# Kernel tuning notes

Measured on AMD Instinct MI355X. Metric: run time of the kernel, lower is better.

Reference implementation:

```python
import jax, jax.numpy as jnp
import numpy as np

DIM = 64
NUM_FEAT = 14
NUM_OUT = 105
N_NODES = 8192
N_EDGES = 16384
N_GRAPHS = 256
N_STEMS = 2048
N_JBONDS = 1024


def lrelu(v):
    return jax.nn.leaky_relu(v, 0.01)


def setup_inputs() -> dict:
    key = jax.random.key(0)
    ks = jax.random.split(key, 40)
    def rn(k, shape, s=0.1):
        return jax.random.normal(k, shape, dtype=jnp.float32) * s
    inp = {}
    inp['x'] = jax.random.normal(ks[0], (N_NODES, NUM_FEAT), dtype=jnp.float32)
    inp['edge_attr'] = jax.random.uniform(ks[1], (N_EDGES, 4), dtype=jnp.float32)
    inp['edge_index'] = jax.random.randint(ks[2], (2, N_EDGES), 0, N_NODES)
    inp['batch'] = jnp.sort(jax.random.randint(ks[3], (N_NODES,), 0, N_GRAPHS))
    inp['stem_atmidx'] = jax.random.randint(ks[4], (N_STEMS,), 0, N_NODES)
    inp['jbond_atmidx'] = jax.random.randint(ks[5], (N_JBONDS, 2), 0, N_NODES)
    # lin0
    inp['lin0_w'] = rn(ks[6], (NUM_FEAT, DIM)); inp['lin0_b'] = rn(ks[7], (DIM,))
    # NNConv edge net: Linear(4,dim) -> LeakyReLU -> Linear(dim, dim*dim)
    inp['net_w1'] = rn(ks[8], (4, DIM)); inp['net_b1'] = rn(ks[9], (DIM,))
    inp['net_w2'] = rn(ks[10], (DIM, DIM * DIM), 0.02); inp['net_b2'] = rn(ks[11], (DIM * DIM,), 0.02)
    # NNConv root weight + bias
    inp['conv_root'] = rn(ks[12], (DIM, DIM)); inp['conv_bias'] = rn(ks[13], (DIM,))
    # GRU (torch gate order r,z,n); stored [in, 3*dim]
    inp['gru_w_ih'] = rn(ks[14], (DIM, 3 * DIM)); inp['gru_w_hh'] = rn(ks[15], (DIM, 3 * DIM))
    inp['gru_b_ih'] = rn(ks[16], (3 * DIM,)); inp['gru_b_hh'] = rn(ks[17], (3 * DIM,))
    # node2stem MLP
    inp['n2s_w1'] = rn(ks[18], (DIM, DIM)); inp['n2s_b1'] = rn(ks[19], (DIM,))
    inp['n2s_w2'] = rn(ks[20], (DIM, NUM_OUT)); inp['n2s_b2'] = rn(ks[21], (NUM_OUT,))
    # node2jbond MLP
    inp['n2j_w1'] = rn(ks[22], (DIM, DIM)); inp['n2j_b1'] = rn(ks[23], (DIM,))
    inp['n2j_w2'] = rn(ks[24], (DIM, 1)); inp['n2j_b2'] = rn(ks[25], (1,))
    # Set2Set LSTM(2*dim -> dim), torch gate order i,f,g,o; stored [in, 4*dim]
    inp['s2s_w_ih'] = rn(ks[26], (2 * DIM, 4 * DIM)); inp['s2s_w_hh'] = rn(ks[27], (DIM, 4 * DIM))
    inp['s2s_b_ih'] = rn(ks[28], (4 * DIM,)); inp['s2s_b_hh'] = rn(ks[29], (4 * DIM,))
    # lin_out
    inp['lin_out_w'] = rn(ks[30], (2 * DIM, 2)); inp['lin_out_b'] = rn(ks[31], (2,))
    return inp


def reference(x, edge_attr, lin0_w, lin0_b, net_w1, net_b1, net_w2, net_b2,
              conv_root, conv_bias, gru_w_ih, gru_w_hh, gru_b_ih, gru_b_hh,
              n2s_w1, n2s_b1, n2s_w2, n2s_b2, n2j_w1, n2j_b1, n2j_w2, n2j_b2,
              s2s_w_ih, s2s_w_hh, s2s_b_ih, s2s_b_hh, lin_out_w, lin_out_b,
              edge_index, batch, stem_atmidx, jbond_atmidx):
    N = x.shape[0]
    src, dst = edge_index[0], edge_index[1]
    out = lrelu(x @ lin0_w + lin0_b)          # [N, dim]
    h = out
    # edge-conditioned weights (edge_attr is constant across the 6 iterations)
    ew = (lrelu(edge_attr @ net_w1 + net_b1) @ net_w2 + net_b2).reshape(-1, DIM, DIM)  # [E,dim,dim]
    deg = jnp.maximum(jax.ops.segment_sum(jnp.ones_like(dst, dtype=x.dtype), dst, num_segments=N), 1.0)[:, None]
    for _ in range(6):
        msg = jnp.einsum('ei,eio->eo', out[src], ew)                        # per-edge matmul
        agg = jax.ops.segment_sum(msg, dst, num_segments=N) / deg          # scatter-mean
        m = lrelu(agg + out @ conv_root + conv_bias)
        # GRU update (torch gate order r,z,n)
        gi = m @ gru_w_ih + gru_b_ih
        gh = h @ gru_w_hh + gru_b_hh
        ir, iz, inn = jnp.split(gi, 3, axis=-1)
        hr, hz, hn = jnp.split(gh, 3, axis=-1)
        r = jax.nn.sigmoid(ir + hr)
        z = jax.nn.sigmoid(iz + hz)
        n = jnp.tanh(inn + r * hn)
        h = (1.0 - z) * n + z * h
        out = h
    # per-stem block logits
    stem_preds = lrelu(out[stem_atmidx] @ n2s_w1 + n2s_b1) @ n2s_w2 + n2s_b2  # [S, num_out]
    # jbond: gather both endpoints, predict scalar, mean over the pair
    jb = out[jbond_atmidx.reshape(-1)]
    jpred = lrelu(jb @ n2j_w1 + n2j_b1) @ n2j_w2 + n2j_b2                     # [2J,1]
    jbond_preds = jpred.reshape(jbond_atmidx.shape).mean(axis=1)              # [J]
    # Set2Set, processing_steps=1
    B = N_GRAPHS
    hS = jnp.zeros((B, DIM), x.dtype)
    cS = jnp.zeros((B, DIM), x.dtype)
    q_star = jnp.zeros((B, 2 * DIM), x.dtype)
    gates = q_star @ s2s_w_ih + s2s_b_ih + hS @ s2s_w_hh + s2s_b_hh
    gi_, gf_, gg_, go_ = jnp.split(gates, 4, axis=-1)
    cS = jax.nn.sigmoid(gf_) * cS + jax.nn.sigmoid(gi_) * jnp.tanh(gg_)
    hS = jax.nn.sigmoid(go_) * jnp.tanh(cS)
    q = hS                                                                    # [B, dim]
    e = jnp.sum(out * q[batch], axis=-1)                                      # [N]
    emax = jax.ops.segment_max(e, batch, num_segments=B)
    a_un = jnp.exp(e - emax[batch])
    a = a_un / jax.ops.segment_sum(a_un, batch, num_segments=B)[batch]
    r_pool = jax.ops.segment_sum(a[:, None] * out, batch, num_segments=B)     # [B, dim]
    q_star = jnp.concatenate([q, r_pool], axis=1)                             # [B, 2*dim]
    scalar_outs = q_star @ lin_out_w + lin_out_b                              # [B, 2]
    return (scalar_outs, stem_preds, jbond_preds)
```

## Files before the change

kernel.cpp:

```cpp
#include <hip/hip_runtime.h>

#define DIM 64
#define NF 14
#define NOUT 105
#define NN 8192
#define NE 16384
#define NB 256
#define NS 2048
#define NJ 1024
#define KTOT 4160

#define C_X      0
#define C_EA     114688
#define C_L0W    180224
#define C_L0B    181120
#define C_NW1    181184
#define C_NB1    181440
#define C_NW2    181504
#define C_NB2    443648
#define C_CRT    447744
#define C_CB     451840
#define C_GWIH   451904
#define C_GWHH   464192
#define C_GBIH   476480
#define C_GBHH   476672
#define C_SW1    476864
#define C_SB1    480960
#define C_SW2    481024
#define C_SB2    487744
#define C_JW1    487856
#define C_JB1    491952
#define C_JW2    492016
#define C_JB2    492080
#define C_S2IH   492088
#define C_S2HH   492344
#define C_LOW    492600
#define C_LOB    492856
#define C_TOT    492864

typedef float f32x4 __attribute__((ext_vector_type(4)));
typedef short bf16x8 __attribute__((ext_vector_type(8)));

__device__ __forceinline__ float bf2f(unsigned short u){
  union { unsigned int i; float f; } v; v.i = ((unsigned int)u) << 16; return v.f;
}
__device__ __forceinline__ unsigned short f2bf(float f){
  union { float f; unsigned int i; } v; v.f = f;
  unsigned int x = v.i;
  return (unsigned short)((x + 0x7FFFu + ((x >> 16) & 1u)) >> 16);
}
__device__ __forceinline__ float sigm(float x){ return 1.f / (1.f + __expf(-x)); }
__device__ __forceinline__ float tanh_f(float x){
  x = fminf(10.f, fmaxf(-10.f, x));
  float e = __expf(2.f * x);
  return (e - 1.f) / (e + 1.f);
}
__device__ __forceinline__ float lrelu(float x){ return x > 0.f ? x : 0.01f * x; }

__device__ __forceinline__ float wred_sum(float v){
  #pragma unroll
  for (int off = 32; off > 0; off >>= 1) v += __shfl_xor(v, off, 64);
  return v;
}
__device__ __forceinline__ float wred_max(float v){
  #pragma unroll
  for (int off = 32; off > 0; off >>= 1) v = fmaxf(v, __shfl_xor(v, off, 64));
  return v;
}


__global__ void k_detect(const unsigned short* __restrict__ ea, int* __restrict__ flag){
  __shared__ int cnt;
  if (threadIdx.x == 0) cnt = 0;
  __syncthreads();
  int c = 0;
  for (int i = threadIdx.x; i < 8192; i += 256) c += (ea[2*i] >> 15) & 1;
  atomicAdd(&cnt, c);
  __syncthreads();
  if (threadIdx.x == 0) *flag = (cnt > 100) ? 1 : 0;
}

struct CvtArgs {
  const void* src[26];
  int n[26];
  int off[26];
};

__global__ void k_cvt(CvtArgs a, const int* __restrict__ flag, unsigned short* __restrict__ dst){
  bool f32 = (*flag != 0);
  int gid = blockIdx.x * blockDim.x + threadIdx.x, gs = gridDim.x * blockDim.x;
  #pragma unroll 1
  for (int j = 0; j < 26; ++j){
    const void* s = a.src[j];
    int n = a.n[j], o = a.off[j];
    for (int i = gid; i < n; i += gs)
      dst[o + i] = f32 ? f2bf(((const float*)s)[i]) : ((const unsigned short*)s)[i];
  }
}

#define SETUP_BLOCKS 7249

__global__ __launch_bounds__(256) void k_setup(const unsigned short* __restrict__ cvt,
                       const int* __restrict__ ei,
                       float* __restrict__ deg,
                       float* __restrict__ actF, unsigned short* __restrict__ actB,
                       unsigned short* __restrict__ z,
                       unsigned short* __restrict__ w2rt,
                       unsigned short* __restrict__ crt, unsigned short* __restrict__ btg,
                       float* __restrict__ cbg, float* __restrict__ qv){
  int bid = blockIdx.x, tid = threadIdx.x;
  if (bid < 2048){
    const unsigned short* x = cvt + C_X;
    const unsigned short* w = cvt + C_L0W;
    const unsigned short* b = cvt + C_L0B;
    int idx = bid * 256 + tid;
    int n = idx >> 6, d = idx & 63;
    float acc = bf2f(b[d]);
    #pragma unroll
    for (int f = 0; f < NF; ++f) acc += bf2f(x[n*NF + f]) * bf2f(w[f*DIM + d]);
    float v = lrelu(acc);
    actF[idx] = v; actB[idx] = f2bf(v);
  } else if (bid < 6144){
    const unsigned short* ea = cvt + C_EA;
    const unsigned short* w  = cvt + C_NW1;
    const unsigned short* b  = cvt + C_NB1;
    int idx = (bid - 2048) * 256 + tid;
    int e = idx >> 6, d = idx & 63;
    float acc = bf2f(b[d]);
    #pragma unroll
    for (int f = 0; f < 4; ++f) acc += bf2f(ea[e*4 + f]) * bf2f(w[f*DIM + d]);
    z[idx] = f2bf(lrelu(acc));
  } else if (bid < 7184){
    int idx = (bid - 6144) * 256 + tid;
    const unsigned short* w2 = cvt + C_NW2;
    const unsigned short* b2 = cvt + C_NB2;
    int o = idx / KTOT, k = idx - o * KTOT;
    w2rt[idx] = (k < 4096) ? w2[(k >> 6) * 4096 + (k & 63) * 64 + o]
                           : b2[(k - 4096) * 64 + o];
  } else if (bid < 7248){
    int e = (bid - 7184) * 256 + tid;
    if (e < NE) atomicAdd(&deg[ei[NE + e]], 1.0f);
  } else {
    const unsigned short* cr  = cvt + C_CRT;
    const unsigned short* wih = cvt + C_GWIH;
    const unsigned short* whh = cvt + C_GWHH;
    const unsigned short* bih = cvt + C_GBIH;
    const unsigned short* bhh = cvt + C_GBHH;
    const unsigned short* s2sbih = cvt + C_S2IH;
    const unsigned short* s2sbhh = cvt + C_S2HH;
    for (int t = tid; t < 4096; t += 256){ int n = t & 63, k = t >> 6; crt[n*64 + k] = cr[k*64 + n]; }
    for (int t = tid; t < 32768; t += 256){
      int nidx = t >> 7, kidx = t & 127;
      int g = nidx >> 6, d = nidx & 63, ki = kidx & 63;
      unsigned short v = 0;
      if (kidx < 64){
        if (g == 0) v = wih[ki*192 + d];
        else if (g == 1) v = wih[ki*192 + 64 + d];
        else if (g == 2) v = wih[ki*192 + 128 + d];
      } else {
        if (g == 0) v = whh[ki*192 + d];
        else if (g == 1) v = whh[ki*192 + 64 + d];
        else if (g == 3) v = whh[ki*192 + 128 + d];
      }
      btg[nidx*128 + kidx] = v;
    }
    if (tid < 256){
      int g = tid >> 6, d = tid & 63;
      float v;
      if (g == 0) v = bf2f(bih[d]) + bf2f(bhh[d]);
      else if (g == 1) v = bf2f(bih[64 + d]) + bf2f(bhh[64 + d]);
      else if (g == 2) v = bf2f(bih[128 + d]);
      else v = bf2f(bhh[128 + d]);
      cbg[tid] = v;
    }
    if (tid < 64){
      float gi = bf2f(s2sbih[tid])       + bf2f(s2sbhh[tid]);
      float gg = bf2f(s2sbih[128 + tid]) + bf2f(s2sbhh[128 + tid]);
      float go = bf2f(s2sbih[192 + tid]) + bf2f(s2sbhh[192 + tid]);
      float c = sigm(gi) * tanh_f(gg);
      qv[tid] = sigm(go) * tanh_f(c);
    }
  }
}


__global__ __launch_bounds__(256) void k_msg(const unsigned short* __restrict__ actB,
                                             const unsigned short* __restrict__ z,
                                             const unsigned short* __restrict__ w2rt,
                                             const int* __restrict__ ei,
                                             float* __restrict__ agg){
  __shared__ float smsg[4 * 2048];
  int tid = threadIdx.x;
  int w = tid >> 6, lane = tid & 63;
  int lm = lane & 15, q8 = (lane >> 4) * 8;
  int e0  = blockIdx.x * 32;
  int kz0 = w * 16;

  uint4 ap[2][2];
  int rowe[2];
  #pragma unroll
  for (int mt = 0; mt < 2; ++mt){
    rowe[mt] = e0 + mt*16 + lm;
    int srcn = ei[rowe[mt]];
    ap[mt][0] = *(const uint4*)&actB[(size_t)srcn*64 + q8];
    ap[mt][1] = *(const uint4*)&actB[(size_t)srcn*64 + 32 + q8];
  }
  const unsigned short* wrow[4];
  #pragma unroll
  for (int nt = 0; nt < 4; ++nt)
    wrow[nt] = w2rt + (size_t)(nt*16 + lm)*KTOT + q8;

  f32x4 acc[2][4];
  #pragma unroll
  for (int mt = 0; mt < 2; ++mt)
    #pragma unroll
    for (int nt = 0; nt < 4; ++nt) acc[mt][nt] = (f32x4){0.f, 0.f, 0.f, 0.f};

  #pragma unroll 4
  for (int u = 0; u < 16; ++u){
    int kz = kz0 + u;
    float zf[2];
    #pragma unroll
    for (int mt = 0; mt < 2; ++mt)
      zf[mt] = bf2f(z[(size_t)rowe[mt]*64 + kz]);
    #pragma unroll
    for (int h = 0; h < 2; ++h){
      bf16x8 bfr[4];
      #pragma unroll
      for (int nt = 0; nt < 4; ++nt)
        bfr[nt] = *(const bf16x8*)&wrow[nt][kz*64 + h*32];
      #pragma unroll
      for (int mt = 0; mt < 2; ++mt){
        const unsigned int* apw = (const unsigned int*)&ap[mt][h];
        bf16x8 af;
        #pragma unroll
        for (int hh = 0; hh < 4; ++hh){
          float flo = __uint_as_float(apw[hh] << 16) * zf[mt];
          float fhi = __uint_as_float(apw[hh] & 0xFFFF0000u) * zf[mt];
          unsigned int pk;
          asm("v_cvt_pk_bf16_f32 %0, %1, %2" : "=v"(pk) : "v"(flo), "v"(fhi));
          ((unsigned int*)&af)[hh] = pk;
        }
        #pragma unroll
        for (int nt = 0; nt < 4; ++nt)
          acc[mt][nt] = __builtin_amdgcn_mfma_f32_16x16x32_bf16(af, bfr[nt], acc[mt][nt], 0, 0, 0);
      }
    }
  }
  if (w == 3){
    #pragma unroll
    for (int h = 0; h < 2; ++h){
      bf16x8 bfr[4];
      #pragma unroll
      for (int nt = 0; nt < 4; ++nt)
        bfr[nt] = *(const bf16x8*)&wrow[nt][4096 + h*32];
      #pragma unroll
      for (int mt = 0; mt < 2; ++mt){
        bf16x8 af = *(const bf16x8*)&ap[mt][h];
        #pragma unroll
        for (int nt = 0; nt < 4; ++nt)
          acc[mt][nt] = __builtin_amdgcn_mfma_f32_16x16x32_bf16(af, bfr[nt], acc[mt][nt], 0, 0, 0);
      }
    }
  }
  {
    int rq = (lane >> 4) * 4;
    float* slab = &smsg[w * 2048];
    #pragma unroll
    for (int mt = 0; mt < 2; ++mt)
      #pragma unroll
      for (int nt = 0; nt < 4; ++nt)
        #pragma unroll
        for (int r = 0; r < 4; ++r)
          slab[(mt*16 + rq + r)*64 + nt*16 + lm] = acc[mt][nt][r];
  }
  __syncthreads();
  for (int idx = tid; idx < 2048; idx += 256){
    int row = idx >> 6, col = idx & 63;
    float s = smsg[idx] + smsg[idx + 2048] + smsg[idx + 4096] + smsg[idx + 6144];
    atomicAdd(&agg[(size_t)ei[NE + e0 + row]*64 + col], s);
  }
}


__global__ __launch_bounds__(256) void k_gru(const unsigned short* __restrict__ actB_in,
                                             const float* __restrict__ actF_in,
                                             float* __restrict__ agg, const float* __restrict__ deg,
                                             const unsigned short* __restrict__ crt,
                                             const unsigned short* __restrict__ cvt,
                                             const unsigned short* __restrict__ btg,
                                             const float* __restrict__ cbg,
                                             float* __restrict__ actF_out, unsigned short* __restrict__ actB_out){
  const unsigned short* cbias = cvt + C_CB;
  __shared__ __align__(16) unsigned short s_frag[2*4*16*8];
  int w = threadIdx.x >> 6, lane = threadIdx.x & 63;
  int lm = lane & 15, q = lane >> 4;
  int q8 = q*8, rq = q*4;
  int r0 = blockIdx.x * 16;
  f32x4 am = (f32x4){0.f, 0.f, 0.f, 0.f};
  #pragma unroll
  for (int kk = 0; kk < 2; ++kk){
    bf16x8 a = *(const bf16x8*)&actB_in[(size_t)(r0 + lm)*64 + kk*32 + q8];
    bf16x8 b = *(const bf16x8*)&crt[(size_t)(w*16 + lm)*64 + kk*32 + q8];
    am = __builtin_amdgcn_mfma_f32_16x16x32_bf16(a, b, am, 0, 0, 0);
  }
  {
    int col = w*16 + lm;
    float cb = bf2f(cbias[col]);
    int kk2 = w >> 1, q2 = (w & 1)*2 + (lm >> 3), j = lm & 7;
    #pragma unroll
    for (int r = 0; r < 4; ++r){
      int row = r0 + rq + r;
      float dg = fmaxf(deg[row], 1.f);
      float v = am[r] + agg[(size_t)row*64 + col] / dg + cb;
      agg[(size_t)row*64 + col] = 0.f;
      s_frag[((kk2*4 + q2)*16 + (rq + r))*8 + j] = f2bf(lrelu(v));
    }
  }
  __syncthreads();
  f32x4 g[4];
  #pragma unroll
  for (int t = 0; t < 4; ++t) g[t] = (f32x4){0.f, 0.f, 0.f, 0.f};
  #pragma unroll
  for (int kk = 0; kk < 4; ++kk){
    bf16x8 a;
    if (kk < 2) a = *(const bf16x8*)&s_frag[(kk*4 + q)*128 + lm*8];
    else        a = *(const bf16x8*)&actB_in[(size_t)(r0 + lm)*64 + (kk - 2)*32 + q8];
    #pragma unroll
    for (int t = 0; t < 4; ++t){
      bf16x8 b = *(const bf16x8*)&btg[(size_t)(t*64 + w*16 + lm)*128 + kk*32 + q8];
      g[t] = __builtin_amdgcn_mfma_f32_16x16x32_bf16(a, b, g[t], 0, 0, 0);
    }
  }
  {
    int d = w*16 + lm;
    float cb_r = cbg[d], cb_z = cbg[64 + d], cb_n = cbg[128 + d], cb_h = cbg[192 + d];
    #pragma unroll
    for (int r = 0; r < 4; ++r){
      int row = r0 + rq + r;
      float rr = sigm(g[0][r] + cb_r);
      float zz = sigm(g[1][r] + cb_z);
      float nn = tanh_f(g[2][r] + cb_n + rr * (g[3][r] + cb_h));
      float ho = actF_in[(size_t)row*64 + d];
      float hn2 = (1.f - zz) * nn + zz * ho;
      actF_out[(size_t)row*64 + d] = hn2;
      actB_out[(size_t)row*64 + d] = f2bf(hn2);
    }
  }
}


__device__ __forceinline__ int lower_bound_batch(const int* b, int val){
  int lo = 0, hi = NN;
  while (lo < hi){ int mid = (lo + hi) >> 1; if (b[mid] < val) lo = mid + 1; else hi = mid; }
  return lo;
}

__device__ __forceinline__ void store_out(void* outp, const int* flag, size_t idx, float v){
  if (*flag) ((float*)outp)[idx] = v;
  else       ((unsigned short*)outp)[idx] = f2bf(v);
}

__global__ __launch_bounds__(256) void k_heads(const float* __restrict__ act,
                                               const int* __restrict__ batch,
                                               const float* __restrict__ qv,
                                               const int* __restrict__ sidx,
                                               const int* __restrict__ jidx,
                                               const unsigned short* __restrict__ cvt,
                                               const int* __restrict__ flag,
                                               void* __restrict__ outp){
  int bid = blockIdx.x;
  int w = threadIdx.x >> 6, lane = threadIdx.x & 63;
  if (bid < 512){
    const unsigned short* w1 = cvt + C_SW1;
    const unsigned short* b1 = cvt + C_SB1;
    const unsigned short* w2 = cvt + C_SW2;
    const unsigned short* b2 = cvt + C_SB2;
    __shared__ float sa[4][64], st[4][64];
    int s = bid * 4 + w;
    int a = sidx[s];
    sa[w][lane] = act[(size_t)a*64 + lane];
    __syncthreads();
    float t = bf2f(b1[lane]);
    #pragma unroll 8
    for (int i = 0; i < 64; ++i) t += sa[w][i] * bf2f(w1[i*64 + lane]);
    st[w][lane] = lrelu(t);
    __syncthreads();
    size_t base = 512 + (size_t)s * NOUT;
    float v = bf2f(b2[lane]);
    #pragma unroll 8
    for (int d = 0; d < 64; ++d) v += st[w][d] * bf2f(w2[d*NOUT + lane]);
    store_out(outp, flag, base + lane, v);
    int o2 = 64 + lane;
    if (o2 < NOUT){
      float v2 = bf2f(b2[o2]);
      #pragma unroll 8
      for (int d = 0; d < 64; ++d) v2 += st[w][d] * bf2f(w2[d*NOUT + o2]);
      store_out(outp, flag, base + o2, v2);
    }
  } else if (bid < 768){
    const unsigned short* w1 = cvt + C_JW1;
    const unsigned short* b1 = cvt + C_JB1;
    const unsigned short* w2 = cvt + C_JW2;
    const unsigned short* b2 = cvt + C_JB2;
    __shared__ float a0[4][64], a1[4][64];
    int j = (bid - 512) * 4 + w;
    int i0 = jidx[j*2], i1 = jidx[j*2 + 1];
    a0[w][lane] = act[(size_t)i0*64 + lane];
    a1[w][lane] = act[(size_t)i1*64 + lane];
    __syncthreads();
    float t0 = bf2f(b1[lane]), t1 = t0;
    #pragma unroll 8
    for (int i = 0; i < 64; ++i){
      float wv = bf2f(w1[i*64 + lane]);
      t0 += a0[w][i] * wv;
      t1 += a1[w][i] * wv;
    }
    t0 = lrelu(t0); t1 = lrelu(t1);
    float p = (t0 + t1) * bf2f(w2[lane]);
    p = wred_sum(p);
    if (lane == 0) store_out(outp, flag, 512 + (size_t)NS*NOUT + j, 0.5f * p + bf2f(b2[0]));
  } else {
    const unsigned short* lw = cvt + C_LOW;
    const unsigned short* lb = cvt + C_LOB;
    __shared__ float se[4][512];
    int b = (bid - 768) * 4 + w;
    int lo = lower_bound_batch(batch, b);
    int hi = lower_bound_batch(batch, b + 1);
    int cnt = hi - lo; if (cnt > 512) cnt = 512;
    float qvl = qv[lane];
    for (int ii = 0; ii < cnt; ++ii){
      float p = act[(size_t)(lo + ii)*64 + lane] * qvl;
      p = wred_sum(p);
      if (lane == 0) se[w][ii] = p;
    }
    __syncthreads();
    float em = -3.4e38f;
    for (int ii = lane; ii < cnt; ii += 64) em = fmaxf(em, se[w][ii]);
    em = wred_max(em);
    float sm = 0.f;
    for (int ii = lane; ii < cnt; ii += 64) sm += __expf(se[w][ii] - em);
    float denom = wred_sum(sm);
    float rp = 0.f;
    for (int ii = 0; ii < cnt; ++ii) rp += __expf(se[w][ii] - em) * act[(size_t)(lo + ii)*64 + lane];
    if (cnt > 0 && denom > 0.f) rp /= denom;
    float s0 = qvl*bf2f(lw[lane*2])     + rp*bf2f(lw[(64 + lane)*2]);
    float s1 = qvl*bf2f(lw[lane*2 + 1]) + rp*bf2f(lw[(64 + lane)*2 + 1]);
    s0 = wred_sum(s0); s1 = wred_sum(s1);
    if (lane == 0){
      store_out(outp, flag, b*2,     s0 + bf2f(lb[0]));
      store_out(outp, flag, b*2 + 1, s1 + bf2f(lb[1]));
    }
  }
}


extern "C" void kernel_launch(void* const* d_in, const int* in_sizes, int n_in,
                              void* d_out, int out_size, void* d_ws, size_t ws_size,
                              hipStream_t stream){
  (void)in_sizes; (void)n_in; (void)out_size; (void)ws_size;
  const int* edge_index = (const int*)d_in[2];
  const int* batch      = (const int*)d_in[3];
  const int* stem_idx   = (const int*)d_in[4];
  const int* jbond_idx  = (const int*)d_in[5];

  char* ws = (char*)d_ws;
  size_t off = 0;
  auto alloc = [&](size_t bytes) -> void* {
    void* p = ws + off; off += (bytes + 255) & ~(size_t)255; return p;
  };
  unsigned short* cvt  = (unsigned short*)alloc((size_t)C_TOT * 2);
  unsigned short* w2rt = (unsigned short*)alloc((size_t)64 * KTOT * 2);
  unsigned short* z_bf = (unsigned short*)alloc((size_t)NE * 64 * 2);
  float* actF0 = (float*)alloc((size_t)NN * 64 * 4);
  float* actF1 = (float*)alloc((size_t)NN * 64 * 4);
  unsigned short* actB0 = (unsigned short*)alloc((size_t)NN * 64 * 2);
  unsigned short* actB1 = (unsigned short*)alloc((size_t)NN * 64 * 2);
  float* deg  = (float*)alloc(NN * 4);
  float* agg  = (float*)alloc((size_t)NN * 64 * 4);
  unsigned short* crt = (unsigned short*)alloc(64 * 64 * 2);
  unsigned short* btg = (unsigned short*)alloc(256 * 128 * 2);
  float* cbg  = (float*)alloc(256 * 4);
  float* qv   = (float*)alloc(64 * 4);
  int* flag   = (int*)alloc(256);

  hipMemsetAsync(deg, 0, ((size_t)NN * 4) + ((size_t)NN * 64 * 4), stream);

  k_detect<<<1, 256, 0, stream>>>((const unsigned short*)d_in[1], flag);

  CvtArgs ca;
  const int srcIdx[26] = {0,1,6,7,8,9,10,11,12,13,14,15,16,17,18,19,20,21,22,23,24,25,28,29,30,31};
  const int ns[26]  = {114688,65536,896,64,256,64,262144,4096,4096,64,12288,12288,192,192,
                       4096,64,6720,105,4096,64,64,1,256,256,256,2};
  const int ofs[26] = {C_X,C_EA,C_L0W,C_L0B,C_NW1,C_NB1,C_NW2,C_NB2,C_CRT,C_CB,C_GWIH,C_GWHH,
                       C_GBIH,C_GBHH,C_SW1,C_SB1,C_SW2,C_SB2,C_JW1,C_JB1,C_JW2,C_JB2,
                       C_S2IH,C_S2HH,C_LOW,C_LOB};
  for (int j = 0; j < 26; ++j){ ca.src[j] = d_in[srcIdx[j]]; ca.n[j] = ns[j]; ca.off[j] = ofs[j]; }
  k_cvt<<<512, 256, 0, stream>>>(ca, flag, cvt);

  k_setup<<<SETUP_BLOCKS, 256, 0, stream>>>(cvt, edge_index, deg,
                                            actF0, actB0, z_bf, w2rt,
                                            crt, btg, cbg, qv);

  for (int t = 0; t < 6; ++t){
    const float* aF_in  = (t & 1) ? actF1 : actF0;
    float* aF_out       = (t & 1) ? actF0 : actF1;
    const unsigned short* aB_in = (t & 1) ? actB1 : actB0;
    unsigned short* aB_out      = (t & 1) ? actB0 : actB1;
    k_msg<<<NE/32, 256, 0, stream>>>(aB_in, z_bf, w2rt, edge_index, agg);
    k_gru<<<NN/16, 256, 0, stream>>>(aB_in, aF_in, agg, deg, crt, cvt, btg, cbg,
                                     aF_out, aB_out);
  }
  k_heads<<<832, 256, 0, stream>>>(actF0, batch, qv, stem_idx, jbond_idx, cvt, flag, d_out);
}
```

Measured before the change: 515.7 us.

## Pre-swizzle edge-net weights into MFMA fragment order and split K across blocks

The setup kernel now lays out the transposed edge-network weight matrix in MFMA B-fragment order, so each lane loads one contiguous 16-byte chunk per fragment instead of strided rows. The message kernel is also split along the K (z-dimension) axis into two halves per 32-edge group, doubling the grid and halving each block's loop. This targets coalescing of weight loads and adds parallelism and occupancy. The cost is that the two K-halves both write into agg, doubling the scatter and atomic traffic in the epilogue.

Result: faster. 470.4 us (-8.8%).

```diff
diff --git a/kernel.cpp b/kernel.cpp
--- a/kernel.cpp
+++ b/kernel.cpp
@@ -105,7 +105,7 @@
                        float* __restrict__ deg,
                        float* __restrict__ actF, unsigned short* __restrict__ actB,
                        unsigned short* __restrict__ z,
-                       unsigned short* __restrict__ w2rt,
+                       unsigned short* __restrict__ w2f,
                        unsigned short* __restrict__ crt, unsigned short* __restrict__ btg,
                        float* __restrict__ cbg, float* __restrict__ qv){
   int bid = blockIdx.x, tid = threadIdx.x;
@@ -134,9 +134,13 @@
     int idx = (bid - 6144) * 256 + tid;
     const unsigned short* w2 = cvt + C_NW2;
     const unsigned short* b2 = cvt + C_NB2;
-    int o = idx / KTOT, k = idx - o * KTOT;
-    w2rt[idx] = (k < 4096) ? w2[(k >> 6) * 4096 + (k & 63) * 64 + o]
-                           : b2[(k - 4096) * 64 + o];
+    int f = idx >> 9, r = idx & 511;
+    int lane = r >> 3, j = r & 7;
+    int kz = f >> 3, h = (f >> 2) & 1, nt = f & 3;
+    int o = nt*16 + (lane & 15);
+    int k = kz*64 + h*32 + (lane >> 4)*8 + j;
+    w2f[idx] = (k < 4096) ? w2[(k >> 6)*4096 + (k & 63)*64 + o]
+                          : b2[(k - 4096)*64 + o];
   } else if (bid < 7248){
     int e = (bid - 7184) * 256 + tid;
     if (e < NE) atomicAdd(&deg[ei[NE + e]], 1.0f);
@@ -186,15 +190,16 @@
 
 __global__ __launch_bounds__(256) void k_msg(const unsigned short* __restrict__ actB,
                                              const unsigned short* __restrict__ z,
-                                             const unsigned short* __restrict__ w2rt,
+                                             const unsigned short* __restrict__ w2f,
                                              const int* __restrict__ ei,
                                              float* __restrict__ agg){
   __shared__ float smsg[4 * 2048];
   int tid = threadIdx.x;
   int w = tid >> 6, lane = tid & 63;
   int lm = lane & 15, q8 = (lane >> 4) * 8;
-  int e0  = blockIdx.x * 32;
-  int kz0 = w * 16;
+  int g  = blockIdx.x >> 1, kh = blockIdx.x & 1;
+  int e0  = g * 32;
+  int kz0 = kh * 32 + w * 8;
 
   uint4 ap[2][2];
   int rowe[2];
@@ -205,10 +210,6 @@
     ap[mt][0] = *(const uint4*)&actB[(size_t)srcn*64 + q8];
     ap[mt][1] = *(const uint4*)&actB[(size_t)srcn*64 + 32 + q8];
   }
-  const unsigned short* wrow[4];
-  #pragma unroll
-  for (int nt = 0; nt < 4; ++nt)
-    wrow[nt] = w2rt + (size_t)(nt*16 + lm)*KTOT + q8;
 
   f32x4 acc[2][4];
   #pragma unroll
@@ -216,8 +217,8 @@
     #pragma unroll
     for (int nt = 0; nt < 4; ++nt) acc[mt][nt] = (f32x4){0.f, 0.f, 0.f, 0.f};
 
-  #pragma unroll 4
-  for (int u = 0; u < 16; ++u){
+  #pragma unroll 2
+  for (int u = 0; u < 8; ++u){
     int kz = kz0 + u;
     float zf[2];
     #pragma unroll
@@ -228,7 +229,7 @@
       bf16x8 bfr[4];
       #pragma unroll
       for (int nt = 0; nt < 4; ++nt)
-        bfr[nt] = *(const bf16x8*)&wrow[nt][kz*64 + h*32];
+        bfr[nt] = *(const bf16x8*)&w2f[(size_t)(kz*8 + h*4 + nt)*512 + lane*8];
       #pragma unroll
       for (int mt = 0; mt < 2; ++mt){
         const unsigned int* apw = (const unsigned int*)&ap[mt][h];
@@ -247,13 +248,13 @@
       }
     }
   }
-  if (w == 3){
+  if (kh == 1 && w == 3){
     #pragma unroll
     for (int h = 0; h < 2; ++h){
       bf16x8 bfr[4];
       #pragma unroll
       for (int nt = 0; nt < 4; ++nt)
-        bfr[nt] = *(const bf16x8*)&wrow[nt][4096 + h*32];
+        bfr[nt] = *(const bf16x8*)&w2f[(size_t)(512 + h*4 + nt)*512 + lane*8];
       #pragma unroll
       for (int mt = 0; mt < 2; ++mt){
         bf16x8 af = *(const bf16x8*)&ap[mt][h];
@@ -470,7 +471,7 @@
     void* p = ws + off; off += (bytes + 255) & ~(size_t)255; return p;
   };
   unsigned short* cvt  = (unsigned short*)alloc((size_t)C_TOT * 2);
-  unsigned short* w2rt = (unsigned short*)alloc((size_t)64 * KTOT * 2);
+  unsigned short* w2f  = (unsigned short*)alloc((size_t)64 * KTOT * 2);
   unsigned short* z_bf = (unsigned short*)alloc((size_t)NE * 64 * 2);
   float* actF0 = (float*)alloc((size_t)NN * 64 * 4);
   float* actF1 = (float*)alloc((size_t)NN * 64 * 4);
@@ -499,7 +500,7 @@
   k_cvt<<<512, 256, 0, stream>>>(ca, flag, cvt);
 
   k_setup<<<SETUP_BLOCKS, 256, 0, stream>>>(cvt, edge_index, deg,
-                                            actF0, actB0, z_bf, w2rt,
+                                            actF0, actB0, z_bf, w2f,
                                             crt, btg, cbg, qv);
 
   for (int t = 0; t < 6; ++t){
@@ -507,7 +508,7 @@
     float* aF_out       = (t & 1) ? actF0 : actF1;
     const unsigned short* aB_in = (t & 1) ? actB1 : actB0;
     unsigned short* aB_out      = (t & 1) ? actB0 : actB1;
-    k_msg<<<NE/32, 256, 0, stream>>>(aB_in, z_bf, w2rt, edge_index, agg);
+    k_msg<<<(NE/32)*2, 256, 0, stream>>>(aB_in, z_bf, w2f, edge_index, agg);
     k_gru<<<NN/16, 256, 0, stream>>>(aB_in, aF_in, agg, deg, crt, cvt, btg, cbg,
                                      aF_out, aB_out);
   }
```
